# Kernel optimization log

Measured on AMD Instinct MI355X. Metric: run time of the kernel, lower is better.

The kernel has to match this reference:

```python
import jax, jax.numpy as jnp
import numpy as np
from jax import lax

B, C, H, W = 64, 256, 32, 32
EPS = 1e-5


def setup_inputs() -> dict:
    key = jax.random.key(0)
    ks = jax.random.split(key, 11)
    c = C
    return {
        "x": jax.random.normal(ks[0], (B, C, H, W), jnp.float32),
        "bn1_gamma": jax.random.uniform(ks[1], (c,), jnp.float32, 0.5, 1.5),
        "bn1_beta": 0.1 * jax.random.normal(ks[2], (c,), jnp.float32),
        "bn1_mean": 0.1 * jax.random.normal(ks[3], (c,), jnp.float32),
        "bn1_var": jax.random.uniform(ks[4], (c,), jnp.float32, 0.5, 1.5),
        "w1": 0.05 * jax.random.normal(ks[5], (c, c, 3, 3), jnp.float32),
        "bn2_gamma": jax.random.uniform(ks[6], (c,), jnp.float32, 0.5, 1.5),
        "bn2_beta": 0.1 * jax.random.normal(ks[7], (c,), jnp.float32),
        "bn2_mean": 0.1 * jax.random.normal(ks[8], (c,), jnp.float32),
        "bn2_var": jax.random.uniform(ks[9], (c,), jnp.float32, 0.5, 1.5),
        "w2": 0.05 * jax.random.normal(ks[10], (c, c, 3, 3), jnp.float32),
    }


def _bn(x, gamma, beta, mean, var):
    # eval-mode BatchNorm2d over channel axis of NCHW
    inv = gamma * lax.rsqrt(var + EPS)
    return x * inv[None, :, None, None] + (beta - mean * inv)[None, :, None, None]


def _binarize(x):
    # TBN binary activations {-1,+1}, straight-through in bwd
    s = jnp.where(x >= 0, 1.0, -1.0).astype(x.dtype)
    return x + lax.stop_gradient(s - x)


def _ternarize(w):
    # TBN ternary weights alpha*{-1,0,+1}; delta = 0.7*mean|W|
    aw = jnp.abs(w)
    delta = 0.7 * jnp.mean(aw)
    mask = (aw > delta).astype(w.dtype)
    alpha = jnp.sum(aw * mask) / jnp.maximum(jnp.sum(mask), 1.0)
    wq = alpha * jnp.sign(w) * mask
    return w + lax.stop_gradient(wq - w)


def _tbn_conv3x3(x, w, stride):
    return lax.conv_general_dilated(
        _binarize(x), _ternarize(w),
        window_strides=(stride, stride), padding=[(1, 1), (1, 1)],
        dimension_numbers=("NCHW", "OIHW", "NCHW"))


def reference(x, bn1_gamma, bn1_beta, bn1_mean, bn1_var, w1,
              bn2_gamma, bn2_beta, bn2_mean, bn2_var, w2):
    identity = x
    h = _tbn_conv3x3(_bn(x, bn1_gamma, bn1_beta, bn1_mean, bn1_var), w1, 1)
    h = _tbn_conv3x3(_bn(h, bn2_gamma, bn2_beta, bn2_mean, bn2_var), w2, 1)
    return identity + h  # ShortCut downsample
```

## Files before the change

### kernel.cpp

```cpp
#include <hip/hip_runtime.h>
#include <stdint.h>


#define EPS 1e-5f

typedef int i32x4  __attribute__((ext_vector_type(4)));
typedef int i32x16 __attribute__((ext_vector_type(16)));

__device__ __forceinline__ void gload16(const void* g, void* l) {
  __builtin_amdgcn_global_load_lds(
      (const __attribute__((address_space(1))) void*)g,
      (__attribute__((address_space(3))) void*)l, 16, 0, 0);
}

__global__ __launch_bounds__(256) void wsum_kernel(const float* __restrict__ w,
                                                   float* __restrict__ partial) {
  __shared__ float red[256];
  const int t = threadIdx.x;
  const int b = blockIdx.x;
  float s = 0.f;
#pragma unroll
  for (int i = 0; i < 32; ++i) s += fabsf(w[b * 256 + t + i * 18432]);
  red[t] = s;
  __syncthreads();
  for (int o = 128; o > 0; o >>= 1) {
    if (t < o) red[t] += red[t + o];
    __syncthreads();
  }
  if (t == 0) partial[b] = red[0];
}

__global__ void delta_kernel(const float* __restrict__ p1, const float* __restrict__ p2,
                             float* __restrict__ delta) {
  const int t = threadIdx.x;
  if (t < 2) {
    const float* p = (t == 0) ? p1 : p2;
    double s = 0.0;
    for (int i = 0; i < 72; ++i) s += (double)p[i];
    delta[t] = 0.7f * (float)(s * (1.0 / 589824.0));
  }
}

__global__ __launch_bounds__(256) void quant_kernel(const float* __restrict__ w,
                                                    const float* __restrict__ delta2, const int didx,
                                                    int8_t* __restrict__ wq,
                                                    float* __restrict__ psum,
                                                    float* __restrict__ pcnt) {
  __shared__ float rs[256];
  __shared__ float rc[256];
  const int t = threadIdx.x;
  const int idx = blockIdx.x * 256 + t;
  const float d = delta2[didx];
  const float v = w[idx];
  const float av = fabsf(v);
  const bool m = av > d;
  const int co = idx / 2304;
  const int rem = idx - co * 2304;
  const int ci = rem / 9;
  const int tap = rem - ci * 9;
  wq[(co >> 6) * 147456 + (ci >> 6) * 36864 + tap * 4096 +
     (((ci & 63) >> 4) << 10) + ((co & 63) << 4) + (ci & 15)] =
      m ? (v > 0.f ? (int8_t)1 : (int8_t)-1) : (int8_t)0;
  rs[t] = m ? av : 0.f;
  rc[t] = m ? 1.f : 0.f;
  __syncthreads();
  for (int o = 128; o > 0; o >>= 1) {
    if (t < o) { rs[t] += rs[t + o]; rc[t] += rc[t + o]; }
    __syncthreads();
  }
  if (t == 0) { psum[blockIdx.x] = rs[0]; pcnt[blockIdx.x] = rc[0]; }
}

__global__ __launch_bounds__(256) void alpha_kernel(const float* __restrict__ ps1, const float* __restrict__ pc1,
                                                    const float* __restrict__ ps2, const float* __restrict__ pc2,
                                                    const float* __restrict__ g2, const float* __restrict__ b2,
                                                    const float* __restrict__ m2, const float* __restrict__ v2,
                                                    float* __restrict__ alphas,
                                                    float* __restrict__ inv2o, float* __restrict__ add2o) {
  __shared__ float rs[256];
  __shared__ float rc[256];
  const int t = threadIdx.x;
  float s1 = 0.f, c1 = 0.f, s2 = 0.f, c2 = 0.f;
#pragma unroll
  for (int i = 0; i < 9; ++i) {
    s1 += ps1[t + (i << 8)]; c1 += pc1[t + (i << 8)];
    s2 += ps2[t + (i << 8)]; c2 += pc2[t + (i << 8)];
  }
  rs[t] = s1; rc[t] = c1;
  __syncthreads();
  for (int o = 128; o > 0; o >>= 1) {
    if (t < o) { rs[t] += rs[t + o]; rc[t] += rc[t + o]; }
    __syncthreads();
  }
  if (t == 0) alphas[0] = rs[0] / fmaxf(rc[0], 1.f);
  __syncthreads();
  rs[t] = s2; rc[t] = c2;
  __syncthreads();
  for (int o = 128; o > 0; o >>= 1) {
    if (t < o) { rs[t] += rs[t + o]; rc[t] += rc[t + o]; }
    __syncthreads();
  }
  if (t == 0) alphas[1] = rs[0] / fmaxf(rc[0], 1.f);
  const float inv = g2[t] * rsqrtf(v2[t] + EPS);
  inv2o[t] = inv;
  add2o[t] = b2[t] - m2[t] * inv;
}

__global__ __launch_bounds__(256) void bn_bin_kernel(const float* __restrict__ x,
                                                     const float* __restrict__ g1,
                                                     const float* __restrict__ b1,
                                                     const float* __restrict__ m1,
                                                     const float* __restrict__ v1,
                                                     int8_t* __restrict__ a1) {
  __shared__ int8_t lds[64 * 40];
  const int t = threadIdx.x;
  const int p0 = blockIdx.x << 6;
  const int c0 = blockIdx.y << 5;
  const int n = blockIdx.z;
  const int pl = t & 63;
  const int cl0 = t >> 6;
#pragma unroll
  for (int i = 0; i < 8; ++i) {
    const int cl = cl0 + (i << 2);
    const int c = c0 + cl;
    const float inv = g1[c] * rsqrtf(v1[c] + EPS);
    const float ad = b1[c] - m1[c] * inv;
    const float val = x[(((n << 8) + c) << 10) + p0 + pl];
    const float tt = fmaf(val, inv, ad);
    lds[pl * 40 + cl] = (tt >= 0.f) ? (int8_t)1 : (int8_t)-1;
  }
  __syncthreads();
  const int pl2 = t >> 2;
  const int s2 = (t & 3) << 3;
  const uint2 o = *(const uint2*)&lds[pl2 * 40 + s2];
  *(uint2*)&a1[(((n << 10) + p0 + pl2) << 8) + c0 + s2] = o;
}

template <int EPI>
__global__ __launch_bounds__(512, 4) void conv3x3_tbn(
    const int8_t* __restrict__ act,
    const int8_t* __restrict__ wq,
    const float* __restrict__ alphas, const int aidx,
    const float* __restrict__ inv2, const float* __restrict__ add2,
    const float* __restrict__ xres,
    int8_t* __restrict__ aout, float* __restrict__ fout) {
  __shared__ int8_t ldsA[4 * 577 * 16];
  __shared__ int8_t ldsB[9 * 4 * 64 * 16];

  const int tid = threadIdx.x;
  const int bid = blockIdx.x;
  const int L = (bid & 7) * 64 + (bid >> 3);
  const int mb = L >> 2;
  const int nb = L & 3;
  const int n = mb >> 1;
  const int y0 = (mb & 1) << 4;
  const int l = tid & 63;
  const int wid = tid >> 6;
  const int lx = l & 31;
  const int lh = l >> 5;

  int srcA[5];
#pragma unroll
  for (int i = 0; i < 5; ++i) {
    const int idx = tid + (i << 9);
    const int asl = idx / 576;
    const int apx = idx - asl * 576;
    int ys = y0 - 1 + (apx >> 5);
    ys = ys < 0 ? 0 : (ys > 31 ? 31 : ys);
    srcA[i] = (((n << 10) + (ys << 5) + (apx & 31)) << 8) + (asl << 4);
  }
  if (tid < 4) *(i32x4*)(ldsA + tid * 9232 + 9216) = (i32x4){0, 0, 0, 0};

  i32x16 acc[2][2];
  acc[0][0] = (i32x16)(0); acc[0][1] = (i32x16)(0);
  acc[1][0] = (i32x16)(0); acc[1][1] = (i32x16)(0);

  const int8_t* wbase = wq + nb * 147456;

#pragma unroll
  for (int i = 0; i < 5; ++i) {
    const int idx = tid + (i << 9);
    if (i < 4 || tid < 256) {
      const int asl = idx / 576;
      const int apx = idx - asl * 576;
      gload16(act + srcA[i], ldsA + asl * 9232 + (apx << 4));
      gload16(wbase + (idx << 4), ldsB + (idx << 4));
    }
  }
  __syncthreads();

  for (int chunk = 0; chunk < 4; ++chunk) {
    __builtin_amdgcn_s_setprio(1);
#pragma unroll
    for (int tap = 0; tap < 9; ++tap) {
      const int ky = tap / 3, kx = tap % 3;
      const int xs = lx + kx - 1;
      const bool xok = (unsigned)xs < 32u;
      int apix[2];
#pragma unroll
      for (int mt = 0; mt < 2; ++mt) {
        const int yr = (wid << 1) + mt + ky;
        const bool ok = xok && ((unsigned)(y0 - 1 + yr) < 32u);
        apix[mt] = ok ? (yr << 5) + xs : 576;
      }
      i32x4 afr[2][2], bfr[2][2];
#pragma unroll
      for (int kh = 0; kh < 2; ++kh) {
        const int sl = lh + (kh << 1);
#pragma unroll
        for (int mt = 0; mt < 2; ++mt)
          afr[mt][kh] = *(const i32x4*)(ldsA + sl * 9232 + (apix[mt] << 4));
#pragma unroll
        for (int nt = 0; nt < 2; ++nt)
          bfr[nt][kh] = *(const i32x4*)(ldsB + (tap << 12) + (sl << 10) + ((nt << 5) + lx) * 16);
      }
#pragma unroll
      for (int mt = 0; mt < 2; ++mt)
#pragma unroll
        for (int nt = 0; nt < 2; ++nt)
#pragma unroll
          for (int kh = 0; kh < 2; ++kh)
            acc[mt][nt] = __builtin_amdgcn_mfma_i32_32x32x32_i8(afr[mt][kh], bfr[nt][kh], acc[mt][nt], 0, 0, 0);
    }
    __builtin_amdgcn_s_setprio(0);
    if (chunk < 3) {
      __syncthreads();
      const int8_t* wch = wbase + (chunk + 1) * 36864;
#pragma unroll
      for (int i = 0; i < 5; ++i) {
        const int idx = tid + (i << 9);
        if (i < 4 || tid < 256) {
          const int asl = idx / 576;
          const int apx = idx - asl * 576;
          gload16(act + srcA[i] + ((chunk + 1) << 6), ldsA + asl * 9232 + (apx << 4));
          gload16(wch + (idx << 4), ldsB + (idx << 4));
        }
      }
      __syncthreads();
    }
  }

  const float alpha = alphas[aidx];
  if constexpr (EPI == 0) {
#pragma unroll
    for (int nt = 0; nt < 2; ++nt) {
      const int co = (nb << 6) + (nt << 5) + lx;
      const float inv = inv2[co];
      const float ad = add2[co];
#pragma unroll
      for (int mt = 0; mt < 2; ++mt) {
        const int pixbase = (mb << 9) + (((wid << 1) + mt) << 5) + (lh << 2);
#pragma unroll
        for (int rg = 0; rg < 16; ++rg) {
          const int pix = pixbase + (rg & 3) + ((rg >> 2) << 3);
          const float h = alpha * (float)acc[mt][nt][rg];
          const float tt = fmaf(h, inv, ad);
          aout[(pix << 8) + co] = (tt >= 0.f) ? (int8_t)1 : (int8_t)-1;
        }
      }
    }
  } else {
#pragma unroll
    for (int nt = 0; nt < 2; ++nt) {
      const int co = (nb << 6) + (nt << 5) + lx;
#pragma unroll
      for (int mt = 0; mt < 2; ++mt) {
        const int pimg0 = ((mb & 1) << 9) + (((wid << 1) + mt) << 5) + (lh << 2);
#pragma unroll
        for (int qd = 0; qd < 4; ++qd) {
          const int off = (((n << 8) + co) << 10) + pimg0 + (qd << 3);
          const float4 xv = *(const float4*)(xres + off);
          float4 o;
          o.x = xv.x + alpha * (float)acc[mt][nt][qd * 4 + 0];
          o.y = xv.y + alpha * (float)acc[mt][nt][qd * 4 + 1];
          o.z = xv.z + alpha * (float)acc[mt][nt][qd * 4 + 2];
          o.w = xv.w + alpha * (float)acc[mt][nt][qd * 4 + 3];
          *(float4*)(fout + off) = o;
        }
      }
    }
  }
}

extern "C" void kernel_launch(void* const* d_in, const int* in_sizes, int n_in,
                              void* d_out, int out_size, void* d_ws, size_t ws_size,
                              hipStream_t stream) {
  const float* x  = (const float*)d_in[0];
  const float* g1 = (const float*)d_in[1];
  const float* b1 = (const float*)d_in[2];
  const float* m1 = (const float*)d_in[3];
  const float* v1 = (const float*)d_in[4];
  const float* w1 = (const float*)d_in[5];
  const float* g2 = (const float*)d_in[6];
  const float* b2 = (const float*)d_in[7];
  const float* m2 = (const float*)d_in[8];
  const float* v2 = (const float*)d_in[9];
  const float* w2 = (const float*)d_in[10];
  float* out = (float*)d_out;

  char* ws = (char*)d_ws;
  int8_t* a1  = (int8_t*)(ws);
  int8_t* a2  = (int8_t*)(ws + 16777216);
  int8_t* wq1 = (int8_t*)(ws + 33554432);
  int8_t* wq2 = (int8_t*)(ws + 33554432 + 589824);
  float* fs = (float*)(ws + 33554432 + 1179648);
  float* pd1    = fs;
  float* pd2    = fs + 128;
  float* deltas = fs + 256;
  float* alphas = fs + 260;
  float* ps1    = fs + 512;
  float* pc1    = fs + 512 + 2304;
  float* ps2    = fs + 512 + 4608;
  float* pc2    = fs + 512 + 6912;
  float* inv2   = fs + 512 + 9216;
  float* add2   = fs + 512 + 9472;

  hipLaunchKernelGGL(wsum_kernel, dim3(72), dim3(256), 0, stream, w1, pd1);
  hipLaunchKernelGGL(wsum_kernel, dim3(72), dim3(256), 0, stream, w2, pd2);
  hipLaunchKernelGGL(delta_kernel, dim3(1), dim3(64), 0, stream, pd1, pd2, deltas);
  hipLaunchKernelGGL(quant_kernel, dim3(2304), dim3(256), 0, stream, w1, deltas, 0, wq1, ps1, pc1);
  hipLaunchKernelGGL(quant_kernel, dim3(2304), dim3(256), 0, stream, w2, deltas, 1, wq2, ps2, pc2);
  hipLaunchKernelGGL(alpha_kernel, dim3(1), dim3(256), 0, stream,
                     ps1, pc1, ps2, pc2, g2, b2, m2, v2, alphas, inv2, add2);
  hipLaunchKernelGGL(bn_bin_kernel, dim3(16, 8, 64), dim3(256), 0, stream, x, g1, b1, m1, v1, a1);
  hipLaunchKernelGGL((conv3x3_tbn<0>), dim3(512), dim3(512), 0, stream,
                     a1, wq1, alphas, 0, inv2, add2, (const float*)nullptr,
                     a2, (float*)nullptr);
  hipLaunchKernelGGL((conv3x3_tbn<1>), dim3(512), dim3(512), 0, stream,
                     a2, wq2, alphas, 1, (const float*)nullptr, (const float*)nullptr, x,
                     (int8_t*)nullptr, out);
  (void)in_sizes; (void)n_in; (void)out_size; (void)ws_size;
}
```

Measured before the change: 132.3 us.

## Double-buffer LDS tiles in TBN conv to overlap next-chunk loads with MFMA

Splits the activation and weight LDS tiles into two buffers each. The async global-to-LDS loads for the next channel chunk are issued before the current chunk's MFMA loop, so that the load latency is hidden behind compute. The barrier-load-barrier sequence between chunks is replaced by one barrier and a buffer swap. This doubles LDS use per block, to roughly 148 KB, and launch bounds drop to one block per CU. That lowers occupancy, and with 512 blocks the grid may now run in more waves.

```diff
diff --git a/kernel.cpp b/kernel.cpp
--- a/kernel.cpp
+++ b/kernel.cpp
@@ -136,16 +136,18 @@
   *(uint2*)&a1[(((n << 10) + p0 + pl2) << 8) + c0 + s2] = o;
 }
 
+#define ABUF 36928
+#define BBUF 36864
 template <int EPI>
-__global__ __launch_bounds__(512, 4) void conv3x3_tbn(
+__global__ __launch_bounds__(512, 1) void conv3x3_tbn(
     const int8_t* __restrict__ act,
     const int8_t* __restrict__ wq,
     const float* __restrict__ alphas, const int aidx,
     const float* __restrict__ inv2, const float* __restrict__ add2,
     const float* __restrict__ xres,
     int8_t* __restrict__ aout, float* __restrict__ fout) {
-  __shared__ int8_t ldsA[4 * 577 * 16];
-  __shared__ int8_t ldsB[9 * 4 * 64 * 16];
+  __shared__ int8_t ldsA[2 * ABUF];
+  __shared__ int8_t ldsB[2 * BBUF];
 
   const int tid = threadIdx.x;
   const int bid = blockIdx.x;
@@ -159,7 +161,7 @@
   const int lx = l & 31;
   const int lh = l >> 5;
 
-  int srcA[5];
+  int srcA[5], dstA[5];
 #pragma unroll
   for (int i = 0; i < 5; ++i) {
     const int idx = tid + (i << 9);
@@ -168,8 +170,9 @@
     int ys = y0 - 1 + (apx >> 5);
     ys = ys < 0 ? 0 : (ys > 31 ? 31 : ys);
     srcA[i] = (((n << 10) + (ys << 5) + (apx & 31)) << 8) + (asl << 4);
-  }
-  if (tid < 4) *(i32x4*)(ldsA + tid * 9232 + 9216) = (i32x4){0, 0, 0, 0};
+    dstA[i] = asl * 9232 + (apx << 4);
+  }
+  if (tid < 8) *(i32x4*)(ldsA + (tid >> 2) * ABUF + (tid & 3) * 9232 + 9216) = (i32x4){0, 0, 0, 0};
 
   i32x16 acc[2][2];
   acc[0][0] = (i32x16)(0); acc[0][1] = (i32x16)(0);
@@ -179,17 +182,32 @@
 
 #pragma unroll
   for (int i = 0; i < 5; ++i) {
-    const int idx = tid + (i << 9);
     if (i < 4 || tid < 256) {
-      const int asl = idx / 576;
-      const int apx = idx - asl * 576;
-      gload16(act + srcA[i], ldsA + asl * 9232 + (apx << 4));
+      gload16(act + srcA[i], ldsA + dstA[i]);
+      const int idx = tid + (i << 9);
       gload16(wbase + (idx << 4), ldsB + (idx << 4));
     }
   }
   __syncthreads();
 
+  int buf = 0;
   for (int chunk = 0; chunk < 4; ++chunk) {
+    const int8_t* aptr = ldsA + buf * ABUF;
+    const int8_t* bptr = ldsB + buf * BBUF;
+    if (chunk < 3) {
+      int8_t* aDst = ldsA + (buf ^ 1) * ABUF;
+      int8_t* bDst = ldsB + (buf ^ 1) * BBUF;
+      const int8_t* wch = wbase + (chunk + 1) * 36864;
+      const int cOff = (chunk + 1) << 6;
+#pragma unroll
+      for (int i = 0; i < 5; ++i) {
+        if (i < 4 || tid < 256) {
+          gload16(act + srcA[i] + cOff, aDst + dstA[i]);
+          const int idx = tid + (i << 9);
+          gload16(wch + (idx << 4), bDst + (idx << 4));
+        }
+      }
+    }
     __builtin_amdgcn_s_setprio(1);
 #pragma unroll
     for (int tap = 0; tap < 9; ++tap) {
@@ -209,10 +227,10 @@
         const int sl = lh + (kh << 1);
 #pragma unroll
         for (int mt = 0; mt < 2; ++mt)
-          afr[mt][kh] = *(const i32x4*)(ldsA + sl * 9232 + (apix[mt] << 4));
+          afr[mt][kh] = *(const i32x4*)(aptr + sl * 9232 + (apix[mt] << 4));
 #pragma unroll
         for (int nt = 0; nt < 2; ++nt)
-          bfr[nt][kh] = *(const i32x4*)(ldsB + (tap << 12) + (sl << 10) + ((nt << 5) + lx) * 16);
+          bfr[nt][kh] = *(const i32x4*)(bptr + (tap << 12) + (sl << 10) + ((nt << 5) + lx) * 16);
       }
 #pragma unroll
       for (int mt = 0; mt < 2; ++mt)
@@ -225,18 +243,7 @@
     __builtin_amdgcn_s_setprio(0);
     if (chunk < 3) {
       __syncthreads();
-      const int8_t* wch = wbase + (chunk + 1) * 36864;
-#pragma unroll
-      for (int i = 0; i < 5; ++i) {
-        const int idx = tid + (i << 9);
-        if (i < 4 || tid < 256) {
-          const int asl = idx / 576;
-          const int apx = idx - asl * 576;
-          gload16(act + srcA[i] + ((chunk + 1) << 6), ldsA + asl * 9232 + (apx << 4));
-          gload16(wch + (idx << 4), ldsB + (idx << 4));
-        }
-      }
-      __syncthreads();
+      buf ^= 1;
     }
   }
 
```

After: 136.0 us. 1.03x slower.
